# Kernel optimization log

Measured on AMD Instinct MI355X. Metric: run time of the kernel, lower is better.

The kernel has to match this reference:

```python
import jax, jax.numpy as jnp
import numpy as np

N = 49998      # num nodes, divisible by (neg_sample_ratio + 2) = 3
E = 800000     # num edges (avg degree 16)
DIM_IN = 128
DIM_OUT = 32
H0 = 8         # heads layer 0
H1 = 1         # heads layer 1


def setup_inputs() -> dict:
    key = jax.random.key(0)
    ks = jax.random.split(key, 16)
    s = 0.05
    x = jax.random.normal(ks[0], (N, DIM_IN), dtype=jnp.float32)
    src = jax.random.randint(ks[1], (E,), 0, N)
    dst = jax.random.randint(ks[2], (E,), 0, N)
    W0 = jax.random.normal(ks[3], (DIM_IN, H0 * DIM_OUT), dtype=jnp.float32) * s
    al0 = jax.random.normal(ks[4], (H0, DIM_OUT), dtype=jnp.float32) * s
    ar0 = jax.random.normal(ks[5], (H0, DIM_OUT), dtype=jnp.float32) * s
    b0 = jnp.zeros((H0 * DIM_OUT,), dtype=jnp.float32)
    W1 = jax.random.normal(ks[6], (H0 * DIM_OUT, H1 * DIM_OUT), dtype=jnp.float32) * s
    al1 = jax.random.normal(ks[7], (H1, DIM_OUT), dtype=jnp.float32) * s
    ar1 = jax.random.normal(ks[8], (H1, DIM_OUT), dtype=jnp.float32) * s
    b1 = jnp.zeros((H1 * DIM_OUT,), dtype=jnp.float32)
    P1 = jax.random.normal(ks[9], (DIM_OUT, DIM_OUT), dtype=jnp.float32) * s
    pb1 = jnp.zeros((DIM_OUT,), dtype=jnp.float32)
    P2 = jax.random.normal(ks[10], (DIM_OUT, DIM_OUT), dtype=jnp.float32) * s
    pb2 = jnp.zeros((DIM_OUT,), dtype=jnp.float32)
    P3 = jax.random.normal(ks[11], (DIM_OUT, 1), dtype=jnp.float32) * s
    pb3 = jnp.zeros((1,), dtype=jnp.float32)
    return dict(x=x, src=src, dst=dst, neg_sample_ratio=1,
                W0=W0, al0=al0, ar0=ar0, b0=b0,
                W1=W1, al1=al1, ar1=ar1, b1=b1,
                P1=P1, pb1=pb1, P2=P2, pb2=pb2, P3=P3, pb3=pb3)


def gat_conv(x, src, dst, W, al, ar, b):
    """DGL GATConv: linear proj -> edge LeakyReLU score -> per-dst segment softmax -> weighted scatter-sum + bias."""
    n = x.shape[0]
    H, D = al.shape
    f = (x @ W).reshape(n, H, D)                     # [N,H,D]
    el = jnp.sum(f * al, axis=-1)                    # [N,H]
    er = jnp.sum(f * ar, axis=-1)                    # [N,H]
    e = jax.nn.leaky_relu(el[src] + er[dst], 0.2)    # [E,H] edge scores
    m = jax.ops.segment_max(e, dst, num_segments=n)  # [N,H] stable softmax max
    a = jnp.exp(e - m[dst])                          # [E,H]
    denom = jax.ops.segment_sum(a, dst, num_segments=n)  # [N,H]
    a = a / denom[dst]                               # normalized attention
    out = jax.ops.segment_sum(a[:, :, None] * f[src], dst, num_segments=n)  # [N,H,D]
    return out + b.reshape(1, H, D)


def reference(x, src, dst, neg_sample_ratio,
              W0, al0, ar0, b0, W1, al1, ar1, b1,
              P1, pb1, P2, pb2, P3, pb3):
    # layer 0: GATConv with ELU activation, flatten heads
    h = jax.nn.elu(gat_conv(x, src, dst, W0, al0, ar0, b0)).reshape(x.shape[0], -1)
    # layer 1: GATConv, no activation, mean over heads
    h = gat_conv(h, src, dst, W1, al1, ar1, b1).mean(axis=1)  # [N, DIM_OUT]

    num_edge = h.shape[0] // (neg_sample_ratio + 2)
    src_h = h[:num_edge]
    pos_dst_h = h[num_edge:2 * num_edge]
    neg_dst_h = h[2 * num_edge:]

    def predictor(z):
        z = jax.nn.relu(z @ P1 + pb1)
        z = jax.nn.relu(z @ P2 + pb2)
        return z @ P3 + pb3

    h_pos = predictor(src_h * pos_dst_h)
    h_neg = predictor(jnp.tile(src_h, (neg_sample_ratio, 1)) * neg_dst_h)
    return (h_pos, h_neg)
```

## Files before the change

### kernel.cpp

```cpp
#include <hip/hip_runtime.h>
#include <hip/hip_fp16.h>
#include <cmath>

#define CAPB 64
#define CAP0 192
#define CAPF 88
#define WA   92
#define G0_ROWS 64
#define G0_PAD 68

typedef _Float16 h2v __attribute__((ext_vector_type(2)));

__device__ __forceinline__ float dot2a(unsigned f, unsigned w, float acc) {
  return __builtin_amdgcn_fdot2(__builtin_bit_cast(h2v, f),
                                __builtin_bit_cast(h2v, w), acc, false);
}
__device__ __forceinline__ unsigned pkh2(float lo, float hi) {
  return (unsigned)__half_as_ushort(__float2half_rn(lo)) |
         ((unsigned)__half_as_ushort(__float2half_rn(hi)) << 16);
}

__global__ void k_gemm0_scatter(const float* __restrict__ x, const float* __restrict__ W0,
                                const float* __restrict__ al, const float* __restrict__ ar,
                                const int* __restrict__ dst, const int* __restrict__ src,
                                const float* __restrict__ W1, unsigned* __restrict__ W1ct,
                                unsigned short* __restrict__ f0h, float* __restrict__ el,
                                float* __restrict__ er, int* __restrict__ cnt,
                                int* __restrict__ ovf_cnt, int* __restrict__ bpad,
                                int* __restrict__ ovf, int N, int E, int ngemm) {
  __shared__ float s_x[128 * G0_PAD];
  int t = threadIdx.x;

  if (blockIdx.x >= ngemm) {
    if (blockIdx.x == ngemm) {
      for (int idx = t; idx < 4096; idx += 256) {
        int c = idx >> 7, k2 = idx & 127;
        float lo = W1[(size_t)(2 * k2) * 32 + c];
        float hi = W1[(size_t)(2 * k2 + 1) * 32 + c];
        W1ct[idx] = pkh2(lo, hi);
      }
    }
    int nscat = gridDim.x - ngemm;
    for (int e = (blockIdx.x - ngemm) * blockDim.x + t; e < E; e += nscat * blockDim.x) {
      int d = dst[e];
      int pos = atomicAdd(&cnt[d], 1);
      if (pos < CAPB) bpad[(size_t)d * CAPB + pos] = src[e];
      else { int op = atomicAdd(ovf_cnt, 1); ovf[op] = e; }
    }
    return;
  }

  int w = t >> 6, l = t & 63;
  int row0 = blockIdx.x * G0_ROWS;
  {
    int row = row0 + l; if (row >= N) row = N - 1;
    const float* xp = x + (size_t)row * 128 + w * 32;
#pragma unroll
    for (int j = 0; j < 8; ++j) {
      float4 v = *(const float4*)(xp + 4 * j);
      int k = w * 32 + 4 * j;
      s_x[(k + 0) * G0_PAD + l] = v.x;
      s_x[(k + 1) * G0_PAD + l] = v.y;
      s_x[(k + 2) * G0_PAD + l] = v.z;
      s_x[(k + 3) * G0_PAD + l] = v.w;
    }
  }
  __syncthreads();

  float4 acc[16];
#pragma unroll
  for (int r = 0; r < 16; ++r) acc[r] = make_float4(0.f, 0.f, 0.f, 0.f);

  const float* wp = W0 + 4 * l;
  int rbase = w * 16;
  for (int k = 0; k < 128; ++k) {
    float4 w4 = *(const float4*)(wp + (size_t)k * 256);
    const float* xk = &s_x[k * G0_PAD + rbase];
    float xv[16];
    *(float4*)&xv[0]  = *(const float4*)(xk);
    *(float4*)&xv[4]  = *(const float4*)(xk + 4);
    *(float4*)&xv[8]  = *(const float4*)(xk + 8);
    *(float4*)&xv[12] = *(const float4*)(xk + 12);
#pragma unroll
    for (int r = 0; r < 16; ++r) {
      acc[r].x = fmaf(xv[r], w4.x, acc[r].x);
      acc[r].y = fmaf(xv[r], w4.y, acc[r].y);
      acc[r].z = fmaf(xv[r], w4.z, acc[r].z);
      acc[r].w = fmaf(xv[r], w4.w, acc[r].w);
    }
  }

  int hh = l >> 3;
  float4 al4 = *(const float4*)(al + 4 * l);
  float4 ar4 = *(const float4*)(ar + 4 * l);
#pragma unroll
  for (int r = 0; r < 16; ++r) {
    int row = row0 + rbase + r;
    float4 f = acc[r];
    if (row < N) {
      ushort4 h4;
      h4.x = __half_as_ushort(__float2half_rn(f.x));
      h4.y = __half_as_ushort(__float2half_rn(f.y));
      h4.z = __half_as_ushort(__float2half_rn(f.z));
      h4.w = __half_as_ushort(__float2half_rn(f.w));
      *(ushort4*)(f0h + (size_t)row * 256 + 4 * l) = h4;
    }
    float pl = fmaf(f.x, al4.x, fmaf(f.y, al4.y, fmaf(f.z, al4.z, f.w * al4.w)));
    float pr = fmaf(f.x, ar4.x, fmaf(f.y, ar4.y, fmaf(f.z, ar4.z, f.w * ar4.w)));
#pragma unroll
    for (int off = 4; off >= 1; off >>= 1) {
      pl += __shfl_xor(pl, off, 64);
      pr += __shfl_xor(pr, off, 64);
    }
    if ((l & 7) == 0 && row < N) {
      el[row * 8 + hh] = pl;
      er[row * 8 + hh] = pr;
    }
  }
}

__global__ void k_fused0(const float* __restrict__ el, const float* __restrict__ er,
                         const unsigned short* __restrict__ f0h, const int* __restrict__ cnt,
                         const int* __restrict__ ovf_cnt, const int* __restrict__ bpad,
                         const int* __restrict__ ovf, const int* __restrict__ dstp,
                         const int* __restrict__ src, const float* __restrict__ b0,
                         const unsigned* __restrict__ W1ct, const float* __restrict__ al1,
                         const float* __restrict__ ar1, float* __restrict__ f1,
                         float* __restrict__ el1, float* __restrict__ er1, int N) {
  __shared__ unsigned s_w1[32 * 132];
  __shared__ unsigned short s_wa[4][8 * WA];
  __shared__ int s_s[4][CAPF];
  __shared__ unsigned s_h2[4][128];

  const int t = threadIdx.x;
  for (int base = t * 4; base < 4096; base += 1024) {
    uint4 v = *(const uint4*)&W1ct[base];
    int c = base >> 7, k2 = base & 127;
    *(uint4*)&s_w1[c * 132 + k2] = v;
  }
  __syncthreads();

  const int w = __builtin_amdgcn_readfirstlane(t >> 6);
  const int l = t & 63;
  const int n = blockIdx.x * 4 + w;
  if (n >= N) return;

  int* sS = s_s[w];
  unsigned short* sWA = s_wa[w];

  const int sub = l & 31, half = l >> 5, hh = sub >> 2;
  float4 b0a = ((const float4*)(b0 + 8 * sub))[0];
  float4 b0b = ((const float4*)(b0 + 8 * sub))[1];
  float al1c = al1[sub], ar1c = ar1[sub];

  int cn = cnt[n];
  int degb = cn < CAPB ? cn : CAPB;
  if (l < degb) sS[l] = bpad[(size_t)n * CAPB + l];
  int deg = degb;
  int ovl = ovf_cnt[0];
  if (ovl) {
    int d = degb;
    if (l == 0) {
      for (int j = 0; j < ovl && d < 84; ++j) {
        int e = ovf[j];
        if (dstp[e] == n) sS[d++] = src[e];
      }
    }
    deg = __shfl(d, 0, 64);
  }

  float er_h = er[n * 8 + (l & 7)];
  float psum = 0.f;
  for (int e = l >> 3; e < deg; e += 8) {
    int sidx = sS[e];
    float v = el[sidx * 8 + (l & 7)] + er_h;
    v = v >= 0.f ? v : 0.2f * v;
    float a = __expf(v);
    sWA[(l & 7) * WA + e] = __half_as_ushort(__float2half_rn(a));
    psum += a;
  }
  psum += __shfl_xor(psum, 8, 64);
  psum += __shfl_xor(psum, 16, 64);
  psum += __shfl_xor(psum, 32, 64);
  float rs = psum > 0.f ? __builtin_amdgcn_rcpf(psum) : 0.f;

  int degp = (deg + 3) & ~3;
  if (l < degp - deg) sS[deg + l] = sS[0];
  { int pe = deg + (l >> 3); if (pe < degp) sWA[(l & 7) * WA + pe] = 0; }

  float a0 = 0.f, a1 = 0.f, a2 = 0.f, a3 = 0.f, a4 = 0.f, a5 = 0.f, a6 = 0.f, a7 = 0.f;
  if (degp > 0) {
    int2 sp = *(const int2*)&sS[2 * half];
    uint4 A = ((const uint4*)(f0h + (size_t)sp.x * 256))[sub];
    uint4 B = ((const uint4*)(f0h + (size_t)sp.y * 256))[sub];
    for (int i = 0;;) {
      int in = i + 4;
      uint4 A2, B2;
      if (in < degp) {
        int2 s2 = *(const int2*)&sS[in + 2 * half];
        A2 = ((const uint4*)(f0h + (size_t)s2.x * 256))[sub];
        B2 = ((const uint4*)(f0h + (size_t)s2.y * 256))[sub];
      }
      unsigned wp = *(const unsigned*)&sWA[hh * WA + i + 2 * half];
      unsigned lo, hi;
      lo = __builtin_amdgcn_perm(A.x, B.x, 0x01000504u);
      hi = __builtin_amdgcn_perm(A.x, B.x, 0x03020706u);
      a0 = dot2a(lo, wp, a0); a1 = dot2a(hi, wp, a1);
      lo = __builtin_amdgcn_perm(A.y, B.y, 0x01000504u);
      hi = __builtin_amdgcn_perm(A.y, B.y, 0x03020706u);
      a2 = dot2a(lo, wp, a2); a3 = dot2a(hi, wp, a3);
      lo = __builtin_amdgcn_perm(A.z, B.z, 0x01000504u);
      hi = __builtin_amdgcn_perm(A.z, B.z, 0x03020706u);
      a4 = dot2a(lo, wp, a4); a5 = dot2a(hi, wp, a5);
      lo = __builtin_amdgcn_perm(A.w, B.w, 0x01000504u);
      hi = __builtin_amdgcn_perm(A.w, B.w, 0x03020706u);
      a6 = dot2a(lo, wp, a6); a7 = dot2a(hi, wp, a7);
      if (in >= degp) break;
      i = in; A = A2; B = B2;
    }
  }
  a0 += __shfl_xor(a0, 32, 64); a1 += __shfl_xor(a1, 32, 64);
  a2 += __shfl_xor(a2, 32, 64); a3 += __shfl_xor(a3, 32, 64);
  a4 += __shfl_xor(a4, 32, 64); a5 += __shfl_xor(a5, 32, 64);
  a6 += __shfl_xor(a6, 32, 64); a7 += __shfl_xor(a7, 32, 64);

  float sc = __shfl(rs, hh, 64);
  float o0 = fmaf(a0, sc, b0a.x), o1 = fmaf(a1, sc, b0a.y);
  float o2 = fmaf(a2, sc, b0a.z), o3 = fmaf(a3, sc, b0a.w);
  float o4 = fmaf(a4, sc, b0b.x), o5 = fmaf(a5, sc, b0b.y);
  float o6 = fmaf(a6, sc, b0b.z), o7 = fmaf(a7, sc, b0b.w);
  o0 = o0 > 0.f ? o0 : expm1f(o0);  o1 = o1 > 0.f ? o1 : expm1f(o1);
  o2 = o2 > 0.f ? o2 : expm1f(o2);  o3 = o3 > 0.f ? o3 : expm1f(o3);
  o4 = o4 > 0.f ? o4 : expm1f(o4);  o5 = o5 > 0.f ? o5 : expm1f(o5);
  o6 = o6 > 0.f ? o6 : expm1f(o6);  o7 = o7 > 0.f ? o7 : expm1f(o7);
  if (half == 0) {
    uint4 hp;
    hp.x = pkh2(o0, o1); hp.y = pkh2(o2, o3);
    hp.z = pkh2(o4, o5); hp.w = pkh2(o6, o7);
    *(uint4*)&s_h2[w][4 * sub] = hp;
  }
  asm volatile("s_waitcnt lgkmcnt(0)" ::: "memory");

  const unsigned* wrow = &s_w1[sub * 132 + half * 64];
  const unsigned* hrow = &s_h2[w][half * 64];
  float p = 0.f;
#pragma unroll
  for (int j = 0; j < 64; j += 4) {
    uint4 wv = *(const uint4*)&wrow[j];
    uint4 hv = *(const uint4*)&hrow[j];
    p = dot2a(hv.x, wv.x, p);
    p = dot2a(hv.y, wv.y, p);
    p = dot2a(hv.z, wv.z, p);
    p = dot2a(hv.w, wv.w, p);
  }
  p += __shfl_xor(p, 32, 64);
  float pl = p * al1c, pr = p * ar1c;
#pragma unroll
  for (int off = 16; off >= 1; off >>= 1) {
    pl += __shfl_xor(pl, off, 64);
    pr += __shfl_xor(pr, off, 64);
  }
  if (half == 0) f1[(size_t)n * 32 + sub] = p;
  if (l == 0) { el1[n] = pl; er1[n] = pr; }
}

__global__ void k_fused1(const float* __restrict__ el, const float* __restrict__ er,
                         const float* __restrict__ f1, const int* __restrict__ cnt,
                         const int* __restrict__ ovf_cnt, const int* __restrict__ bpad,
                         const int* __restrict__ ovf, const int* __restrict__ dstp,
                         const int* __restrict__ src, const float* __restrict__ b1,
                         float* __restrict__ h1, int N) {
  __shared__ float s_w[4][CAP0];
  __shared__ int s_s[4][CAP0];
  int g = threadIdx.x >> 6;
  int lane = threadIdx.x & 63;
  int n = blockIdx.x * 4 + g;
  int nn = n < N ? n : N - 1;
  int cn = cnt[nn];
  int degb = cn < CAPB ? cn : CAPB;
  float er_n = er[nn];

  for (int i = lane; i < degb; i += 64)
    s_s[g][i] = bpad[(size_t)nn * CAPB + i];
  int deg = degb;
  {
    int ovl = ovf_cnt[0];
    if (ovl) {
      if (lane == 0) {
        int d = degb;
        for (int j = 0; j < ovl && d < CAP0; ++j) {
          int e = ovf[j];
          if (dstp[e] == nn) s_s[g][d++] = src[e];
        }
        s_w[g][0] = __int_as_float(d);
      }
      deg = __float_as_int(__shfl(s_w[g][0], 0, 64));
    }
  }

  float m = -INFINITY;
  for (int i = lane; i < deg; i += 64) {
    float v = el[s_s[g][i]] + er_n;
    v = v >= 0.f ? v : 0.2f * v;
    s_w[g][i] = v;
    m = fmaxf(m, v);
  }
#pragma unroll
  for (int off = 32; off >= 1; off >>= 1) m = fmaxf(m, __shfl_xor(m, off, 64));
  float sum = 0.f;
  for (int i = lane; i < deg; i += 64) {
    float a = expf(s_w[g][i] - m);
    s_w[g][i] = a;
    sum += a;
  }
#pragma unroll
  for (int off = 32; off >= 1; off >>= 1) sum += __shfl_xor(sum, off, 64);
  for (int i = lane; i < deg; i += 64) s_w[g][i] /= sum;

  int es = lane >> 3, q = lane & 7;
  float4 a4 = make_float4(0.f, 0.f, 0.f, 0.f);
  int i = es;
  for (; i + 8 < deg; i += 16) {
    float a = s_w[g][i];
    float b = s_w[g][i + 8];
    float4 v0 = ((const float4*)(f1 + (size_t)s_s[g][i] * 32))[q];
    float4 v1 = ((const float4*)(f1 + (size_t)s_s[g][i + 8] * 32))[q];
    a4.x = fmaf(a, v0.x, a4.x); a4.y = fmaf(a, v0.y, a4.y);
    a4.z = fmaf(a, v0.z, a4.z); a4.w = fmaf(a, v0.w, a4.w);
    a4.x = fmaf(b, v1.x, a4.x); a4.y = fmaf(b, v1.y, a4.y);
    a4.z = fmaf(b, v1.z, a4.z); a4.w = fmaf(b, v1.w, a4.w);
  }
  for (; i < deg; i += 8) {
    float a = s_w[g][i];
    float4 v = ((const float4*)(f1 + (size_t)s_s[g][i] * 32))[q];
    a4.x = fmaf(a, v.x, a4.x); a4.y = fmaf(a, v.y, a4.y);
    a4.z = fmaf(a, v.z, a4.z); a4.w = fmaf(a, v.w, a4.w);
  }
#pragma unroll
  for (int off = 8; off <= 32; off <<= 1) {
    a4.x += __shfl_xor(a4.x, off, 64);
    a4.y += __shfl_xor(a4.y, off, 64);
    a4.z += __shfl_xor(a4.z, off, 64);
    a4.w += __shfl_xor(a4.w, off, 64);
  }
  if (lane < 8 && n < N) {
    float4 b = *(const float4*)(b1 + lane * 4);
    a4.x += b.x; a4.y += b.y; a4.z += b.z; a4.w += b.w;
    ((float4*)(h1 + (size_t)n * 32))[lane] = a4;
  }
}

__global__ void k_pred(const float* __restrict__ h1, const float* __restrict__ P1,
                       const float* __restrict__ pb1, const float* __restrict__ P2,
                       const float* __restrict__ pb2, const float* __restrict__ P3,
                       const float* __restrict__ pb3, float* __restrict__ out,
                       int num_edge, int total) {
  int t = threadIdx.x;
  int lane = t & 31, grp = t >> 5;
  int k = blockIdx.x * 8 + grp;
  int kk = k < total ? k : 0;
  float z;
  if (kk < num_edge) {
    z = h1[(size_t)kk * 32 + lane] * h1[(size_t)(kk + num_edge) * 32 + lane];
  } else {
    int i = kk - num_edge;
    z = h1[(size_t)(i % num_edge) * 32 + lane] * h1[(size_t)(2 * num_edge + i) * 32 + lane];
  }
  double a1 = 0;
#pragma unroll
  for (int d = 0; d < 32; ++d)
    a1 += (double)__shfl(z, d, 32) * (double)P1[d * 32 + lane];
  float t1 = (float)(a1 + (double)pb1[lane]);
  t1 = t1 > 0.f ? t1 : 0.f;
  double a2 = 0;
#pragma unroll
  for (int d = 0; d < 32; ++d)
    a2 += (double)__shfl(t1, d, 32) * (double)P2[d * 32 + lane];
  float t2 = (float)(a2 + (double)pb2[lane]);
  t2 = t2 > 0.f ? t2 : 0.f;
  double a3 = (double)t2 * (double)P3[lane];
#pragma unroll
  for (int off = 16; off >= 1; off >>= 1) a3 += __shfl_xor(a3, off, 64);
  if (lane == 0 && k < total) out[k] = (float)(a3 + (double)pb3[0]);
}

extern "C" void kernel_launch(void* const* d_in, const int* in_sizes, int n_in,
                              void* d_out, int out_size, void* d_ws, size_t ws_size,
                              hipStream_t stream) {
  const float* x   = (const float*)d_in[0];
  const int*   src = (const int*)d_in[1];
  const int*   dst = (const int*)d_in[2];
  const float* W0  = (const float*)d_in[4];
  const float* al0 = (const float*)d_in[5];
  const float* ar0 = (const float*)d_in[6];
  const float* b0  = (const float*)d_in[7];
  const float* W1  = (const float*)d_in[8];
  const float* al1 = (const float*)d_in[9];
  const float* ar1 = (const float*)d_in[10];
  const float* b1  = (const float*)d_in[11];
  const float* P1  = (const float*)d_in[12];
  const float* pb1 = (const float*)d_in[13];
  const float* P2  = (const float*)d_in[14];
  const float* pb2 = (const float*)d_in[15];
  const float* P3  = (const float*)d_in[16];
  const float* pb3 = (const float*)d_in[17];

  int N = in_sizes[0] / 128;
  int E = in_sizes[1];
  int num_edge = N - out_size;

  size_t off = 0;
  auto alloc = [&](size_t bytes) -> void* {
    void* p = (char*)d_ws + off;
    off += (bytes + 255) & ~(size_t)255;
    return p;
  };
  unsigned short* f0h = (unsigned short*)alloc((size_t)N * 256 * 2);
  float* f1   = (float*)alloc((size_t)N * 32 * 4);
  float* h1   = (float*)alloc((size_t)N * 32 * 4);
  float* el   = (float*)alloc((size_t)N * 8 * 4);
  float* er   = (float*)alloc((size_t)N * 8 * 4);
  float* el1  = (float*)alloc((size_t)N * 4);
  float* er1  = (float*)alloc((size_t)N * 4);
  int*   cnt  = (int*)alloc((size_t)(N + 1) * 4);
  int*   bpad = (int*)alloc((size_t)N * CAPB * 4);
  int*   ovf  = (int*)alloc((size_t)E * 4);
  unsigned* W1ct = (unsigned*)alloc(4096 * 4);
  if (off > ws_size) return;
  int* ovf_cnt = cnt + N;

  int ngemm = (N + G0_ROWS - 1) / G0_ROWS;
  hipMemsetAsync(cnt, 0, (size_t)(N + 1) * 4, stream);
  k_gemm0_scatter<<<1792, 256, 0, stream>>>(x, W0, al0, ar0, dst, src, W1, W1ct,
                                            f0h, el, er, cnt, ovf_cnt, bpad, ovf,
                                            N, E, ngemm);
  k_fused0<<<(N + 3) / 4, 256, 0, stream>>>(el, er, f0h, cnt, ovf_cnt, bpad, ovf, dst,
                                            src, b0, W1ct, al1, ar1, f1, el1, er1, N);
  k_fused1<<<(N + 3) / 4, 256, 0, stream>>>(el1, er1, f1, cnt, ovf_cnt, bpad, ovf, dst,
                                            src, b1, h1, N);
  k_pred<<<(out_size + 7) / 8, 256, 0, stream>>>(h1, P1, pb1, P2, pb2, P3, pb3,
                                                 (float*)d_out, num_edge, out_size);
}
```

Measured before the change: 283.6 us.

## Use fp16 dot2 for layer-0 GEMM and fp16 features in layer-1 aggregation

Adds a prep kernel that packs W0 and W1 into fp16 pairs, and switches the layer-0 projection from fp32 FMAs to packed fp16 dot2 instructions. The x tile is staged in shared memory as packed halves. Layer-1 features f1 are stored as fp16, and k_fused1 is rewritten to skip the max-subtraction pass, pack attention weights in fp16, and accumulate with dot2 and a single reciprocal normalization. This cuts ALU work and gather bandwidth but lowers precision. Dropping the softmax max-shift risks overflow, and the overflow edge list is now capped at a smaller size.

```diff
diff --git a/kernel.cpp b/kernel.cpp
--- a/kernel.cpp
+++ b/kernel.cpp
@@ -3,8 +3,8 @@
 #include <cmath>
 
 #define CAPB 64
-#define CAP0 192
 #define CAPF 88
+#define CAP1 96
 #define WA   92
 #define G0_ROWS 64
 #define G0_PAD 68
@@ -20,26 +20,30 @@
          ((unsigned)__half_as_ushort(__float2half_rn(hi)) << 16);
 }
 
-__global__ void k_gemm0_scatter(const float* __restrict__ x, const float* __restrict__ W0,
+__global__ void k_prep(const float* __restrict__ W0, const float* __restrict__ W1,
+                       unsigned* __restrict__ W0h, unsigned* __restrict__ W1ct) {
+  int idx = blockIdx.x * 256 + threadIdx.x;
+  if (idx < 16384) {
+    int k2 = idx >> 8, c = idx & 255;
+    W0h[idx] = pkh2(W0[(size_t)(2 * k2) * 256 + c], W0[(size_t)(2 * k2 + 1) * 256 + c]);
+  } else if (idx < 20480) {
+    int j = idx - 16384;
+    int c = j >> 7, k2 = j & 127;
+    W1ct[j] = pkh2(W1[(size_t)(2 * k2) * 32 + c], W1[(size_t)(2 * k2 + 1) * 32 + c]);
+  }
+}
+
+__global__ void k_gemm0_scatter(const float* __restrict__ x, const unsigned* __restrict__ W0h,
                                 const float* __restrict__ al, const float* __restrict__ ar,
                                 const int* __restrict__ dst, const int* __restrict__ src,
-                                const float* __restrict__ W1, unsigned* __restrict__ W1ct,
                                 unsigned short* __restrict__ f0h, float* __restrict__ el,
                                 float* __restrict__ er, int* __restrict__ cnt,
                                 int* __restrict__ ovf_cnt, int* __restrict__ bpad,
                                 int* __restrict__ ovf, int N, int E, int ngemm) {
-  __shared__ float s_x[128 * G0_PAD];
+  __shared__ unsigned s_x2[64 * G0_PAD];
   int t = threadIdx.x;
 
   if (blockIdx.x >= ngemm) {
-    if (blockIdx.x == ngemm) {
-      for (int idx = t; idx < 4096; idx += 256) {
-        int c = idx >> 7, k2 = idx & 127;
-        float lo = W1[(size_t)(2 * k2) * 32 + c];
-        float hi = W1[(size_t)(2 * k2 + 1) * 32 + c];
-        W1ct[idx] = pkh2(lo, hi);
-      }
-    }
     int nscat = gridDim.x - ngemm;
     for (int e = (blockIdx.x - ngemm) * blockDim.x + t; e < E; e += nscat * blockDim.x) {
       int d = dst[e];
@@ -58,11 +62,9 @@
 #pragma unroll
     for (int j = 0; j < 8; ++j) {
       float4 v = *(const float4*)(xp + 4 * j);
-      int k = w * 32 + 4 * j;
-      s_x[(k + 0) * G0_PAD + l] = v.x;
-      s_x[(k + 1) * G0_PAD + l] = v.y;
-      s_x[(k + 2) * G0_PAD + l] = v.z;
-      s_x[(k + 3) * G0_PAD + l] = v.w;
+      int k2 = w * 16 + 2 * j;
+      s_x2[k2 * G0_PAD + l] = pkh2(v.x, v.y);
+      s_x2[(k2 + 1) * G0_PAD + l] = pkh2(v.z, v.w);
     }
   }
   __syncthreads();
@@ -71,22 +73,22 @@
 #pragma unroll
   for (int r = 0; r < 16; ++r) acc[r] = make_float4(0.f, 0.f, 0.f, 0.f);
 
-  const float* wp = W0 + 4 * l;
+  const unsigned* wp = W0h + 4 * l;
   int rbase = w * 16;
-  for (int k = 0; k < 128; ++k) {
-    float4 w4 = *(const float4*)(wp + (size_t)k * 256);
-    const float* xk = &s_x[k * G0_PAD + rbase];
-    float xv[16];
-    *(float4*)&xv[0]  = *(const float4*)(xk);
-    *(float4*)&xv[4]  = *(const float4*)(xk + 4);
-    *(float4*)&xv[8]  = *(const float4*)(xk + 8);
-    *(float4*)&xv[12] = *(const float4*)(xk + 12);
+  for (int k2 = 0; k2 < 64; ++k2) {
+    uint4 w4 = *(const uint4*)(wp + (size_t)k2 * 256);
+    const unsigned* xk = &s_x2[k2 * G0_PAD + rbase];
+    unsigned xv[16];
+    *(uint4*)&xv[0]  = *(const uint4*)(xk);
+    *(uint4*)&xv[4]  = *(const uint4*)(xk + 4);
+    *(uint4*)&xv[8]  = *(const uint4*)(xk + 8);
+    *(uint4*)&xv[12] = *(const uint4*)(xk + 12);
 #pragma unroll
     for (int r = 0; r < 16; ++r) {
-      acc[r].x = fmaf(xv[r], w4.x, acc[r].x);
-      acc[r].y = fmaf(xv[r], w4.y, acc[r].y);
-      acc[r].z = fmaf(xv[r], w4.z, acc[r].z);
-      acc[r].w = fmaf(xv[r], w4.w, acc[r].w);
+      acc[r].x = dot2a(xv[r], w4.x, acc[r].x);
+      acc[r].y = dot2a(xv[r], w4.y, acc[r].y);
+      acc[r].z = dot2a(xv[r], w4.z, acc[r].z);
+      acc[r].w = dot2a(xv[r], w4.w, acc[r].w);
     }
   }
 
@@ -125,7 +127,7 @@
                          const int* __restrict__ ovf, const int* __restrict__ dstp,
                          const int* __restrict__ src, const float* __restrict__ b0,
                          const unsigned* __restrict__ W1ct, const float* __restrict__ al1,
-                         const float* __restrict__ ar1, float* __restrict__ f1,
+                         const float* __restrict__ ar1, unsigned short* __restrict__ f1h,
                          float* __restrict__ el1, float* __restrict__ er1, int N) {
   __shared__ unsigned s_w1[32 * 132];
   __shared__ unsigned short s_wa[4][8 * WA];
@@ -254,99 +256,99 @@
     p = dot2a(hv.w, wv.w, p);
   }
   p += __shfl_xor(p, 32, 64);
+  float pn = __shfl_xor(p, 1, 64);
   float pl = p * al1c, pr = p * ar1c;
 #pragma unroll
   for (int off = 16; off >= 1; off >>= 1) {
     pl += __shfl_xor(pl, off, 64);
     pr += __shfl_xor(pr, off, 64);
   }
-  if (half == 0) f1[(size_t)n * 32 + sub] = p;
+  if (half == 0 && (sub & 1) == 0)
+    *(unsigned*)(f1h + (size_t)n * 32 + sub) = pkh2(p, pn);
   if (l == 0) { el1[n] = pl; er1[n] = pr; }
 }
 
 __global__ void k_fused1(const float* __restrict__ el, const float* __restrict__ er,
-                         const float* __restrict__ f1, const int* __restrict__ cnt,
+                         const unsigned short* __restrict__ f1h, const int* __restrict__ cnt,
                          const int* __restrict__ ovf_cnt, const int* __restrict__ bpad,
                          const int* __restrict__ ovf, const int* __restrict__ dstp,
                          const int* __restrict__ src, const float* __restrict__ b1,
                          float* __restrict__ h1, int N) {
-  __shared__ float s_w[4][CAP0];
-  __shared__ int s_s[4][CAP0];
-  int g = threadIdx.x >> 6;
-  int lane = threadIdx.x & 63;
+  __shared__ int s_s[4][CAP1];
+  __shared__ unsigned s_wp[4][CAP1 / 2];
+
+  const int t = threadIdx.x;
+  const int g = __builtin_amdgcn_readfirstlane(t >> 6);
+  const int lane = t & 63;
   int n = blockIdx.x * 4 + g;
   int nn = n < N ? n : N - 1;
+  int* sS = s_s[g];
+  unsigned* sWP = s_wp[g];
+
   int cn = cnt[nn];
   int degb = cn < CAPB ? cn : CAPB;
+  if (lane < degb) sS[lane] = bpad[(size_t)nn * CAPB + lane];
+  int deg = degb;
+  int ovl = ovf_cnt[0];
+  if (ovl) {
+    int d = degb;
+    if (lane == 0) {
+      for (int j = 0; j < ovl && d < CAP1 - 16; ++j) {
+        int e = ovf[j];
+        if (dstp[e] == nn) sS[d++] = src[e];
+      }
+    }
+    deg = __shfl(d, 0, 64);
+  }
   float er_n = er[nn];
-
-  for (int i = lane; i < degb; i += 64)
-    s_s[g][i] = bpad[(size_t)nn * CAPB + i];
-  int deg = degb;
-  {
-    int ovl = ovf_cnt[0];
-    if (ovl) {
-      if (lane == 0) {
-        int d = degb;
-        for (int j = 0; j < ovl && d < CAP0; ++j) {
-          int e = ovf[j];
-          if (dstp[e] == nn) s_s[g][d++] = src[e];
-        }
-        s_w[g][0] = __int_as_float(d);
-      }
-      deg = __float_as_int(__shfl(s_w[g][0], 0, 64));
-    }
-  }
-
-  float m = -INFINITY;
-  for (int i = lane; i < deg; i += 64) {
-    float v = el[s_s[g][i]] + er_n;
-    v = v >= 0.f ? v : 0.2f * v;
-    s_w[g][i] = v;
-    m = fmaxf(m, v);
-  }
-#pragma unroll
-  for (int off = 32; off >= 1; off >>= 1) m = fmaxf(m, __shfl_xor(m, off, 64));
-  float sum = 0.f;
-  for (int i = lane; i < deg; i += 64) {
-    float a = expf(s_w[g][i] - m);
-    s_w[g][i] = a;
-    sum += a;
-  }
-#pragma unroll
-  for (int off = 32; off >= 1; off >>= 1) sum += __shfl_xor(sum, off, 64);
-  for (int i = lane; i < deg; i += 64) s_w[g][i] /= sum;
-
-  int es = lane >> 3, q = lane & 7;
-  float4 a4 = make_float4(0.f, 0.f, 0.f, 0.f);
-  int i = es;
-  for (; i + 8 < deg; i += 16) {
-    float a = s_w[g][i];
-    float b = s_w[g][i + 8];
-    float4 v0 = ((const float4*)(f1 + (size_t)s_s[g][i] * 32))[q];
-    float4 v1 = ((const float4*)(f1 + (size_t)s_s[g][i + 8] * 32))[q];
-    a4.x = fmaf(a, v0.x, a4.x); a4.y = fmaf(a, v0.y, a4.y);
-    a4.z = fmaf(a, v0.z, a4.z); a4.w = fmaf(a, v0.w, a4.w);
-    a4.x = fmaf(b, v1.x, a4.x); a4.y = fmaf(b, v1.y, a4.y);
-    a4.z = fmaf(b, v1.z, a4.z); a4.w = fmaf(b, v1.w, a4.w);
-  }
-  for (; i < deg; i += 8) {
-    float a = s_w[g][i];
-    float4 v = ((const float4*)(f1 + (size_t)s_s[g][i] * 32))[q];
-    a4.x = fmaf(a, v.x, a4.x); a4.y = fmaf(a, v.y, a4.y);
-    a4.z = fmaf(a, v.z, a4.z); a4.w = fmaf(a, v.w, a4.w);
+  int degp = (deg + 15) & ~15;
+  asm volatile("s_waitcnt lgkmcnt(0)" ::: "memory");
+  if (deg + lane < degp) sS[deg + lane] = sS[0];
+
+  float psum = 0.f;
+  for (int i0 = 0; i0 < degp; i0 += 64) {
+    int i = i0 + lane;
+    float a = 0.f;
+    if (i < deg) {
+      float v = el[sS[i]] + er_n;
+      v = v >= 0.f ? v : 0.2f * v;
+      a = __expf(v);
+      psum += a;
+    }
+    float an = __shfl_xor(a, 8, 64);
+    if ((lane & 15) < 8 && i < degp)
+      sWP[(i0 >> 1) + ((lane >> 4) << 3) + (lane & 7)] = pkh2(a, an);
+  }
+#pragma unroll
+  for (int off = 32; off >= 1; off >>= 1) psum += __shfl_xor(psum, off, 64);
+  float rs = psum > 0.f ? __builtin_amdgcn_rcpf(psum) : 0.f;
+
+  asm volatile("s_waitcnt lgkmcnt(0)" ::: "memory");
+  const int es = lane >> 3, q = lane & 7;
+  float c0 = 0.f, c1 = 0.f, c2 = 0.f, c3 = 0.f;
+  for (int i0 = 0; i0 < degp; i0 += 16) {
+    int sA = sS[i0 + es], sB = sS[i0 + es + 8];
+    uint2 A = *(const uint2*)(f1h + (size_t)sA * 32 + 4 * q);
+    uint2 B = *(const uint2*)(f1h + (size_t)sB * 32 + 4 * q);
+    unsigned wp = sWP[(i0 >> 1) + es];
+    unsigned lo = __builtin_amdgcn_perm(A.x, B.x, 0x01000504u);
+    unsigned hi = __builtin_amdgcn_perm(A.x, B.x, 0x03020706u);
+    c0 = dot2a(lo, wp, c0); c1 = dot2a(hi, wp, c1);
+    lo = __builtin_amdgcn_perm(A.y, B.y, 0x01000504u);
+    hi = __builtin_amdgcn_perm(A.y, B.y, 0x03020706u);
+    c2 = dot2a(lo, wp, c2); c3 = dot2a(hi, wp, c3);
   }
 #pragma unroll
   for (int off = 8; off <= 32; off <<= 1) {
-    a4.x += __shfl_xor(a4.x, off, 64);
-    a4.y += __shfl_xor(a4.y, off, 64);
-    a4.z += __shfl_xor(a4.z, off, 64);
-    a4.w += __shfl_xor(a4.w, off, 64);
-  }
-  if (lane < 8 && n < N) {
-    float4 b = *(const float4*)(b1 + lane * 4);
-    a4.x += b.x; a4.y += b.y; a4.z += b.z; a4.w += b.w;
-    ((float4*)(h1 + (size_t)n * 32))[lane] = a4;
+    c0 += __shfl_xor(c0, off, 64); c1 += __shfl_xor(c1, off, 64);
+    c2 += __shfl_xor(c2, off, 64); c3 += __shfl_xor(c3, off, 64);
+  }
+  if (es == 0 && n < N) {
+    float4 b = *(const float4*)(b1 + 4 * q);
+    float4 o;
+    o.x = fmaf(c0, rs, b.x); o.y = fmaf(c1, rs, b.y);
+    o.z = fmaf(c2, rs, b.z); o.w = fmaf(c3, rs, b.w);
+    ((float4*)(h1 + (size_t)n * 32))[q] = o;
   }
 }
 
@@ -416,7 +418,7 @@
     return p;
   };
   unsigned short* f0h = (unsigned short*)alloc((size_t)N * 256 * 2);
-  float* f1   = (float*)alloc((size_t)N * 32 * 4);
+  unsigned short* f1h = (unsigned short*)alloc((size_t)N * 32 * 2);
   float* h1   = (float*)alloc((size_t)N * 32 * 4);
   float* el   = (float*)alloc((size_t)N * 8 * 4);
   float* er   = (float*)alloc((size_t)N * 8 * 4);
@@ -426,17 +428,19 @@
   int*   bpad = (int*)alloc((size_t)N * CAPB * 4);
   int*   ovf  = (int*)alloc((size_t)E * 4);
   unsigned* W1ct = (unsigned*)alloc(4096 * 4);
+  unsigned* W0h  = (unsigned*)alloc(16384 * 4);
   if (off > ws_size) return;
   int* ovf_cnt = cnt + N;
 
   int ngemm = (N + G0_ROWS - 1) / G0_ROWS;
   hipMemsetAsync(cnt, 0, (size_t)(N + 1) * 4, stream);
-  k_gemm0_scatter<<<1792, 256, 0, stream>>>(x, W0, al0, ar0, dst, src, W1, W1ct,
+  k_prep<<<80, 256, 0, stream>>>(W0, W1, W0h, W1ct);
+  k_gemm0_scatter<<<1792, 256, 0, stream>>>(x, W0h, al0, ar0, dst, src,
                                             f0h, el, er, cnt, ovf_cnt, bpad, ovf,
                                             N, E, ngemm);
   k_fused0<<<(N + 3) / 4, 256, 0, stream>>>(el, er, f0h, cnt, ovf_cnt, bpad, ovf, dst,
-                                            src, b0, W1ct, al1, ar1, f1, el1, er1, N);
-  k_fused1<<<(N + 3) / 4, 256, 0, stream>>>(el1, er1, f1, cnt, ovf_cnt, bpad, ovf, dst,
+                                            src, b0, W1ct, al1, ar1, f1h, el1, er1, N);
+  k_fused1<<<(N + 3) / 4, 256, 0, stream>>>(el1, er1, f1h, cnt, ovf_cnt, bpad, ovf, dst,
                                             src, b1, h1, N);
   k_pred<<<(out_size + 7) / 8, 256, 0, stream>>>(h1, P1, pb1, P2, pb2, P3, pb3,
                                                  (float*)d_out, num_edge, out_size);
```

New measurement: 297.2 us. +4.8%, slower.
